# Kernel optimization log

Measured on AMD Instinct MI355X. Metric: run time of the kernel, lower is better.

## Reference

```python
import jax, jax.numpy as jnp
import numpy as np

H = 16      # how_many_heads
DH = 64     # dimension_of_head
D_K = 1024  # dimension_of_key (input dim); scaler = sqrt(D_K), faithful to source
NEG = -np.finfo(np.float32).max


def setup_inputs() -> dict:
    key0 = jax.random.key(0)
    ks = jax.random.split(key0, 8)
    B, S, D = 2, 2048, 1024
    query = jax.random.normal(ks[0], (B, S, D), dtype=jnp.float32)
    key_in = jax.random.normal(ks[1], (B, S, D), dtype=jnp.float32)
    value = jax.random.normal(ks[2], (B, S, D), dtype=jnp.float32)
    mask = jax.random.bernoulli(ks[3], 0.5, (B, S, S))  # bool, True = masked
    # nn.Linear(in, out, bias=False): y = x @ W^T with W:[out,in]; store [in,out] directly
    sc = 1.0 / np.sqrt(D)
    W_q = jax.random.normal(ks[4], (D, H * DH), dtype=jnp.float32) * sc
    W_k = jax.random.normal(ks[5], (D, H * DH), dtype=jnp.float32) * sc
    W_v = jax.random.normal(ks[6], (D, H * DH), dtype=jnp.float32) * sc
    W_o = jax.random.normal(ks[7], (H * DH, D), dtype=jnp.float32) * sc
    return {"query": query, "key": key_in, "value": value, "mask": mask,
            "W_q": W_q, "W_k": W_k, "W_v": W_v, "W_o": W_o}


def reference(query, key, value, mask, W_q, W_k, W_v, W_o):
    B, Sq, _ = query.shape
    # project and split heads: [B, S, H, DH] -> [B, H, S, DH]
    q = (query @ W_q).reshape(B, Sq, H, DH).transpose(0, 2, 1, 3)
    k = (key @ W_k).reshape(B, -1, H, DH).transpose(0, 2, 1, 3)
    v = (value @ W_v).reshape(B, -1, H, DH).transpose(0, 2, 1, 3)
    # scores: [B, H, Sq, Sk], scaled by sqrt(dimension_of_key)=sqrt(D_K)
    scores = jnp.einsum('bhqd,bhkd->bhqk', q, k) / np.float32(np.sqrt(D_K))
    # mask: [B, Sq, Sk] -> [B, H, Sq, Sk]; masked_fill with -finfo(float32).max
    scores = jnp.where(mask[:, None, :, :], NEG, scores)
    # FAITHFUL to source: softmax over dim=2 (the QUERY axis of the 4D tensor)
    attn = jax.nn.softmax(scores, axis=2)
    hidden = jnp.einsum('bhqk,bhkd->bhqd', attn, v)  # [B, H, Sq, DH]
    hidden = hidden.transpose(0, 2, 1, 3).reshape(B, Sq, H * DH) @ W_o
    return hidden, k, v
```

## Files before the change

kernel.cpp:

```cpp
#include <hip/hip_runtime.h>
#include <hip/hip_bf16.h>

#define BB 2
#define SS 2048
#define DD 1024
#define HH 16
#define DHH 64

#define SCLOG2E 0.045084221f

typedef unsigned short u16;
typedef unsigned int   u32;
typedef __bf16 bf16_t;
typedef bf16_t bf16x8 __attribute__((ext_vector_type(8)));
typedef u16    u16x8  __attribute__((ext_vector_type(8)));
typedef u32    u32x4v __attribute__((ext_vector_type(4)));
typedef float  f32x4  __attribute__((ext_vector_type(4)));

#define MFMA(a,b,c) __builtin_amdgcn_mfma_f32_16x16x32_bf16(a,b,c,0,0,0)

#define SW(c,r)  ((c) ^ ((r) & 7))
#define SW3(c,r) ((c) ^ ((r) & 3))

typedef __attribute__((address_space(1))) const unsigned int as1_u32;
typedef __attribute__((address_space(3))) unsigned int as3_u32;

__device__ __forceinline__ void gld16(const void* g, void* l){
  __builtin_amdgcn_global_load_lds((as1_u32*)g, (as3_u32*)l, 16, 0, 0);
}

__device__ __forceinline__ u16 f2bf(float f){
  u32 u = __builtin_bit_cast(u32, f);
  u32 r = (u + 0x7fffu + ((u >> 16) & 1u)) >> 16;
  return (u16)r;
}
__device__ __forceinline__ u16 nbf(float f){
  bf16_t b = (bf16_t)f;
  return __builtin_bit_cast(u16, b);
}
__device__ __forceinline__ float bf2f(u16 v){
  u32 u = ((u32)v) << 16;
  return __builtin_bit_cast(float, u);
}
__device__ __forceinline__ bf16x8 ldb8(const u16* p){
  return __builtin_bit_cast(bf16x8, *(const u16x8*)p);
}

__device__ __forceinline__ void stage64(const u16* __restrict__ g0, int stride,
                                        u16* lds0, int tid){
  int w = tid >> 6, lane = tid & 63;
  #pragma unroll
  for (int j = 0; j < 2; j++){
    int slot = j*256 + w*64 + lane;
    int row = slot >> 3, c = slot & 7;
    gld16(g0 + (size_t)row*stride + (SW(c,row) << 3),
          lds0 + (size_t)(j*256 + w*64)*8);
  }
}

__device__ __forceinline__ void stage32(const u16* __restrict__ g0, int stride,
                                        u16* lds0, int tid){
  int w = tid >> 6, lane = tid & 63;
  #pragma unroll
  for (int j = 0; j < 2; j++){
    int slot = j*256 + w*64 + lane;
    int row = slot >> 2, c = slot & 3;
    gld16(g0 + (size_t)row*stride + (SW3(c,row) << 3),
          lds0 + (size_t)(j*256 + w*64)*8);
  }
}

__global__ __launch_bounds__(256) void cvt3(const float* __restrict__ s0,
                                            const float* __restrict__ s1,
                                            const float* __restrict__ s2,
                                            u16* __restrict__ d0,
                                            u16* __restrict__ d1,
                                            u16* __restrict__ d2){
  const float* s = blockIdx.z == 0 ? s0 : (blockIdx.z == 1 ? s1 : s2);
  u16*         d = blockIdx.z == 0 ? d0 : (blockIdx.z == 1 ? d1 : d2);
  size_t i = ((size_t)blockIdx.x*256 + threadIdx.x) * 8;
  const float4* p = (const float4*)(s + i);
  float4 x = p[0], y = p[1];
  u16x8 u;
  u[0]=f2bf(x.x); u[1]=f2bf(x.y); u[2]=f2bf(x.z); u[3]=f2bf(x.w);
  u[4]=f2bf(y.x); u[5]=f2bf(y.y); u[6]=f2bf(y.z); u[7]=f2bf(y.w);
  *(u16x8*)(d + i) = u;
}

__global__ __launch_bounds__(256) void detect_mask(const u32* mw, u32* flag){
  __shared__ int fBig, fFloat;
  if (threadIdx.x == 0){ fBig = 0; fFloat = 0; }
  __syncthreads();
  for (int i = threadIdx.x; i < 4096; i += 256){
    u32 w = mw[i];
    if (w == 0x3f800000u) fFloat = 1;
    else if (w > 1u) fBig = 1;
  }
  __syncthreads();
  if (threadIdx.x == 0) *flag = fFloat ? 2u : (fBig ? 1u : 0u);
}

__global__ __launch_bounds__(256) void pack_mask(const void* __restrict__ mask,
                                                 const u32* __restrict__ flag,
                                                 u32* __restrict__ pm){
  int w = blockIdx.x * 256 + threadIdx.x;
  if (w >= BB*SS*(SS/32)) return;
  u32 f = *flag;
  size_t e0 = (size_t)w * 32;
  u32 bits = 0;
  if (f == 1u){
    const uchar4* mb = (const uchar4*)((const unsigned char*)mask + e0);
    #pragma unroll
    for (int j = 0; j < 8; j++){
      uchar4 v = mb[j];
      bits |= (v.x?1u:0u) << (4*j)   | (v.y?1u:0u) << (4*j+1)
            | (v.z?1u:0u) << (4*j+2) | (v.w?1u:0u) << (4*j+3);
    }
  } else if (f == 0u){
    const int4* mi = (const int4*)((const int*)mask + e0);
    #pragma unroll
    for (int j = 0; j < 8; j++){
      int4 v = mi[j];
      bits |= (v.x?1u:0u) << (4*j)   | (v.y?1u:0u) << (4*j+1)
            | (v.z?1u:0u) << (4*j+2) | (v.w?1u:0u) << (4*j+3);
    }
  } else {
    const float4* mf = (const float4*)((const float*)mask + e0);
    #pragma unroll
    for (int j = 0; j < 8; j++){
      float4 v = mf[j];
      bits |= (v.x!=0.f?1u:0u) << (4*j)   | (v.y!=0.f?1u:0u) << (4*j+1)
            | (v.z!=0.f?1u:0u) << (4*j+2) | (v.w!=0.f?1u:0u) << (4*j+3);
    }
  }
  pm[w] = bits;
}

__global__ __launch_bounds__(256) void prep_w(const float* __restrict__ W0,
                                              const float* __restrict__ W1,
                                              const float* __restrict__ W2,
                                              const float* __restrict__ W3,
                                              u16* __restrict__ Wt){
  const float* Ws[4] = {W0, W1, W2, W3};
  const float* W = Ws[blockIdx.z];
  float scl = (blockIdx.z == 0) ? SCLOG2E : 1.0f;
  u16* O = Wt + (size_t)blockIdx.z * DD * DD;
  __shared__ float tile[64][65];
  int kb = blockIdx.x * 64, nb = blockIdx.y * 64;
  int col = threadIdx.x & 63, rr = threadIdx.x >> 6;
  #pragma unroll
  for (int i = 0; i < 16; i++){
    int row = i*4 + rr;
    tile[row][col] = W[(size_t)(kb+row)*DD + nb + col];
  }
  __syncthreads();
  #pragma unroll
  for (int i = 0; i < 16; i++){
    int row = i*4 + rr;
    O[(size_t)(nb+row)*DD + kb + col] = f2bf(tile[col][row] * scl);
  }
}

struct GA { const u16* A; const u16* Bt; u16* Cb; float* Co; int mode; };

__global__ __launch_bounds__(256) void gemm32(GA a0, GA a1, GA a2){
  GA ga = blockIdx.z == 0 ? a0 : (blockIdx.z == 1 ? a1 : a2);
  __shared__ u16 As[2][128*32];
  __shared__ u16 Bs[2][128*32];
  int mb = blockIdx.x * 128, nb = blockIdx.y * 128;
  int tid = threadIdx.x, w = tid >> 6, lane = tid & 63, ln = lane & 15, g = lane >> 4;
  int wr = w >> 1, wc = w & 1;
  f32x4 acc[4][4];
  #pragma unroll
  for (int i = 0; i < 4; i++)
    #pragma unroll
    for (int j = 0; j < 4; j++) acc[i][j] = (f32x4){0,0,0,0};

  stage32(ga.A  + (size_t)mb*DD, DD, As[0], tid);
  stage32(ga.Bt + (size_t)nb*DD, DD, Bs[0], tid);
  __syncthreads();
  int buf = 0;
  for (int t = 0; t < 32; t++){
    if (t < 31){
      stage32(ga.A  + (size_t)mb*DD + (t+1)*32, DD, As[buf^1], tid);
      stage32(ga.Bt + (size_t)nb*DD + (t+1)*32, DD, Bs[buf^1], tid);
    }
    bf16x8 av[4], bv[4];
    #pragma unroll
    for (int mf = 0; mf < 4; mf++){
      int row = wr*64 + mf*16 + ln;
      av[mf] = ldb8(&As[buf][row*32 + (SW3(g,row) << 3)]);
    }
    #pragma unroll
    for (int nf = 0; nf < 4; nf++){
      int row = wc*64 + nf*16 + ln;
      bv[nf] = ldb8(&Bs[buf][row*32 + (SW3(g,row) << 3)]);
    }
    #pragma unroll
    for (int mf = 0; mf < 4; mf++)
      #pragma unroll
      for (int nf = 0; nf < 4; nf++)
        acc[mf][nf] = MFMA(av[mf], bv[nf], acc[mf][nf]);
    __syncthreads();
    buf ^= 1;
  }
  #pragma unroll
  for (int mf = 0; mf < 4; mf++){
    #pragma unroll
    for (int nf = 0; nf < 4; nf++){
      #pragma unroll
      for (int r = 0; r < 4; r++){
        int row = mb + wr*64 + mf*16 + g*4 + r;
        int col = nb + wc*64 + nf*16 + ln;
        float v = acc[mf][nf][r];
        if (ga.mode != 2)
          ga.Cb[(size_t)row*DD + col] = f2bf(v);
        if (ga.mode == 1){
          int b_ = row >> 11, s_ = row & (SS-1);
          int h_ = col >> 6,  d_ = col & 63;
          ga.Co[(((size_t)(b_*HH + h_))*SS + s_)*DHH + d_] = v;
        }
        if (ga.mode == 2)
          ga.Co[(size_t)row*DD + col] = v;
      }
    }
  }
}

__global__ __launch_bounds__(256) void pass1_sum(const u16* __restrict__ Qb,
                                                 const u16* __restrict__ Kb,
                                                 const u32* __restrict__ pm,
                                                 float* __restrict__ cO){
  __shared__ u16 Qst[2][64*64];
  int b = blockIdx.z, h = blockIdx.y;
  int kblk = blockIdx.x * 128;
  int tid = threadIdx.x, w = tid >> 6, lane = tid & 63, ln = lane & 15, g = lane >> 4;
  bf16x8 kf[2][2];
  #pragma unroll
  for (int f = 0; f < 2; f++){
    const u16* kp = Kb + ((size_t)b*SS + kblk + w*32 + f*16 + ln)*DD + h*DHH + g*8;
    kf[f][0] = ldb8(kp); kf[f][1] = ldb8(kp + 32);
  }
  float cr[2][4] = {{0,0,0,0},{0,0,0,0}};

  stage64(Qb + ((size_t)b*SS)*DD + h*DHH, DD, Qst[0], tid);
  __syncthreads();
  int buf = 0;
  int kwbase = (b*SS)*(SS/32) + (kblk >> 5) + w;
  for (int t = 0; t < 32; t++){
    if (t < 31) stage64(Qb + ((size_t)b*SS + (t+1)*64)*DD + h*DHH, DD, Qst[buf^1], tid);
    #pragma unroll
    for (int qc = 0; qc < 4; qc++){
      int row = qc*16 + ln;
      bf16x8 b0 = ldb8(&Qst[buf][row*64 + (SW(g,  row) << 3)]);
      bf16x8 b1 = ldb8(&Qst[buf][row*64 + (SW(g+4,row) << 3)]);
      int q = t*64 + qc*16 + ln;
      u32 mw = pm[(size_t)q*(SS/32) + kwbase];
      #pragma unroll
      for (int f = 0; f < 2; f++){
        f32x4 sf = {0,0,0,0};
        sf = MFMA(kf[f][0], b0, sf);
        sf = MFMA(kf[f][1], b1, sf);
        #pragma unroll
        for (int r = 0; r < 4; r++){
          float e = __builtin_amdgcn_exp2f(sf[r]);
          cr[f][r] += ((mw >> (f*16 + g*4 + r)) & 1u) ? 0.f : e;
        }
      }
    }
    __syncthreads();
    buf ^= 1;
  }
  #pragma unroll
  for (int f = 0; f < 2; f++)
    #pragma unroll
    for (int r = 0; r < 4; r++){
      #pragma unroll
      for (int msk = 1; msk < 16; msk <<= 1)
        cr[f][r] += __shfl_xor(cr[f][r], msk, 64);
    }
  if (ln == 0){
    #pragma unroll
    for (int f = 0; f < 2; f++)
      #pragma unroll
      for (int r = 0; r < 4; r++)
        cO[((size_t)b*HH + h)*SS + kblk + w*32 + f*16 + g*4 + r] = cr[f][r];
  }
}

__global__ __launch_bounds__(256) void scale_v(const u16* __restrict__ Vb,
                                               const float* __restrict__ cI,
                                               u16* __restrict__ Vt){
  int b = blockIdx.z, h = blockIdx.y;
  int st = blockIdx.x * 64;
  __shared__ u16 tile[64][72];
  int col = threadIdx.x & 63, rr = threadIdx.x >> 6;
  #pragma unroll
  for (int i = 0; i < 16; i++){
    int row = i*4 + rr;
    int s = st + row;
    float inv = 1.0f / cI[((size_t)b*HH + h)*SS + s];
    float v = bf2f(Vb[((size_t)b*SS + s)*DD + h*DHH + col]);
    tile[row][col] = f2bf(v * inv);
  }
  __syncthreads();
  int pc = ((col >> 2) & 3)*16 + (col >> 4)*4 + (col & 3);
  #pragma unroll
  for (int i = 0; i < 16; i++){
    int row = i*4 + rr;
    Vt[(((size_t)b*HH + h)*DHH + row)*SS + st + pc] = tile[col][row];
  }
}

__global__ __launch_bounds__(256) void pass2_pv(const u16* __restrict__ Qb,
                                                const u16* __restrict__ Kb,
                                                const u16* __restrict__ Vt,
                                                const u32* __restrict__ pm,
                                                u16* __restrict__ Hb){
  __shared__ u16 Kst[2][64*64];
  __shared__ u16 Vst[2][64*64];
  __shared__ u16 P[4][32*72];
  int b = blockIdx.z, h = blockIdx.y;
  int qt = blockIdx.x * 128;
  int tid = threadIdx.x, w = tid >> 6, lane = tid & 63, ln = lane & 15, g = lane >> 4;
  u16* Pw = &P[w][0];
  bf16x8 qf[2][2];
  #pragma unroll
  for (int f = 0; f < 2; f++){
    const u16* qp = Qb + ((size_t)b*SS + qt + w*32 + f*16 + ln)*DD + h*DHH + g*8;
    qf[f][0] = ldb8(qp); qf[f][1] = ldb8(qp + 32);
  }
  f32x4 acc[2][4];
  #pragma unroll
  for (int f = 0; f < 2; f++)
    #pragma unroll
    for (int d = 0; d < 4; d++) acc[f][d] = (f32x4){0,0,0,0};

  const u16* Kg  = Kb + ((size_t)b*SS)*DD + h*DHH;
  const u16* Vth = Vt + ((size_t)b*HH + h)*DHH*SS;

  stage64(Kg,  DD, Kst[0], tid);
  stage64(Vth, SS, Vst[0], tid);
  __syncthreads();
  int buf = 0;
  for (int t = 0; t < 32; t++){
    if (t < 31){
      stage64(Kg + (size_t)(t+1)*64*DD, DD, Kst[buf^1], tid);
      stage64(Vth + (t+1)*64,           SS, Vst[buf^1], tid);
    }
    u32 mlo[2], mhi[2];
    #pragma unroll
    for (int f = 0; f < 2; f++){
      const u32* pw = pm + ((size_t)b*SS + qt + w*32 + f*16 + ln)*(SS/32) + t*2;
      mlo[f] = pw[0]; mhi[f] = pw[1];
    }
    u32 pk[2][8];
    #pragma unroll
    for (int kc = 0; kc < 4; kc++){
      int row = kc*16 + ln;
      bf16x8 a0 = ldb8(&Kst[buf][row*64 + (SW(g,  row) << 3)]);
      bf16x8 a1 = ldb8(&Kst[buf][row*64 + (SW(g+4,row) << 3)]);
      #pragma unroll
      for (int f = 0; f < 2; f++){
        f32x4 sf = {0,0,0,0};
        sf = MFMA(a0, qf[f][0], sf);
        sf = MFMA(a1, qf[f][1], sf);
        u32 mword = (kc < 2) ? mlo[f] : mhi[f];
        int msh = (kc & 1) * 16 + g*4;
        float p0 = ((mword >> (msh+0)) & 1u) ? 0.f : __builtin_amdgcn_exp2f(sf[0]);
        float p1 = ((mword >> (msh+1)) & 1u) ? 0.f : __builtin_amdgcn_exp2f(sf[1]);
        float p2 = ((mword >> (msh+2)) & 1u) ? 0.f : __builtin_amdgcn_exp2f(sf[2]);
        float p3 = ((mword >> (msh+3)) & 1u) ? 0.f : __builtin_amdgcn_exp2f(sf[3]);
        pk[f][kc*2]   = (u32)nbf(p0) | ((u32)nbf(p1) << 16);
        pk[f][kc*2+1] = (u32)nbf(p2) | ((u32)nbf(p3) << 16);
      }
    }
    #pragma unroll
    for (int f = 0; f < 2; f++){
      u16* pr = &Pw[(f*16 + ln)*72 + g*16];
      *(u32x4v*)pr       = (u32x4v){pk[f][0], pk[f][1], pk[f][2], pk[f][3]};
      *(u32x4v*)(pr + 8) = (u32x4v){pk[f][4], pk[f][5], pk[f][6], pk[f][7]};
    }
    #pragma unroll
    for (int kh = 0; kh < 2; kh++){
      bf16x8 pa[2];
      #pragma unroll
      for (int f = 0; f < 2; f++)
        pa[f] = ldb8(&Pw[(f*16 + ln)*72 + kh*32 + g*8]);
      #pragma unroll
      for (int df = 0; df < 4; df++){
        int row = df*16 + ln;
        bf16x8 bv = ldb8(&Vst[buf][row*64 + (SW(kh*4+g, row) << 3)]);
        #pragma unroll
        for (int f = 0; f < 2; f++)
          acc[f][df] = MFMA(pa[f], bv, acc[f][df]);
      }
    }
    __syncthreads();
    buf ^= 1;
  }
  #pragma unroll
  for (int f = 0; f < 2; f++)
    #pragma unroll
    for (int df = 0; df < 4; df++)
      #pragma unroll
      for (int r = 0; r < 4; r++){
        int row = qt + w*32 + f*16 + g*4 + r;
        int col = h*DHH + df*16 + ln;
        Hb[((size_t)b*SS + row)*DD + col] = f2bf(acc[f][df][r]);
      }
}

extern "C" void kernel_launch(void* const* d_in, const int* in_sizes, int n_in,
                              void* d_out, int out_size, void* d_ws, size_t ws_size,
                              hipStream_t stream){
  (void)in_sizes; (void)n_in; (void)out_size; (void)ws_size;
  const float* query = (const float*)d_in[0];
  const float* key   = (const float*)d_in[1];
  const float* value = (const float*)d_in[2];
  const void*  mask  = d_in[3];
  const float* W_q = (const float*)d_in[4];
  const float* W_k = (const float*)d_in[5];
  const float* W_v = (const float*)d_in[6];
  const float* W_o = (const float*)d_in[7];

  float* out   = (float*)d_out;
  float* out_h = out;
  float* out_k = out   + (size_t)BB*HH*SS*DHH;
  float* out_v = out_k + (size_t)BB*HH*SS*DHH;

  char* w = (char*)d_ws;
  u16*   Wt  = (u16*)(w);
  u16*   Av  = (u16*)(w + (size_t)( 8u<<20));
  u16*   Qb  = (u16*)(w + (size_t)(16u<<20));
  u16*   Kb  = (u16*)(w + (size_t)(24u<<20));
  u16*   Vb  = (u16*)(w + (size_t)(32u<<20));
  u16*   Vt  = (u16*)(w + (size_t)(40u<<20));
  float* cS  = (float*)(w + (size_t)(48u<<20));
  u32*   pm  = (u32*)(w + (size_t)(48u<<20) + (512u<<10));
  u32*   flag= (u32*)(w + (size_t)(48u<<20) + (1664u<<10));
  u16*   Hb  = Av;
  u16*   Aq  = (u16*)out_h;
  u16*   Ak  = Aq + (size_t)BB*SS*DD;

  detect_mask<<<dim3(1), dim3(256), 0, stream>>>((const u32*)mask, flag);
  pack_mask<<<dim3(1024), dim3(256), 0, stream>>>(mask, flag, pm);
  prep_w<<<dim3(16,16,4), dim3(256), 0, stream>>>(W_q, W_k, W_v, W_o, Wt);

  cvt3<<<dim3(2048,1,3), dim3(256), 0, stream>>>(query, key, value, Aq, Ak, Av);

  GA gq = { Aq, Wt,             Qb, nullptr, 0 };
  GA gk = { Ak, Wt + 1*1048576, Kb, out_k,   1 };
  GA gv = { Av, Wt + 2*1048576, Vb, out_v,   1 };
  gemm32<<<dim3(32,8,3), dim3(256), 0, stream>>>(gq, gk, gv);

  pass1_sum<<<dim3(SS/128, HH, BB), dim3(256), 0, stream>>>(Qb, Kb, pm, cS);
  scale_v<<<dim3(SS/64, HH, BB), dim3(256), 0, stream>>>(Vb, cS, Vt);
  pass2_pv<<<dim3(SS/128, HH, BB), dim3(256), 0, stream>>>(Qb, Kb, Vt, pm, Hb);

  GA go = { Hb, Wt + 3*1048576, nullptr, out_h, 2 };
  gemm32<<<dim3(32,8,1), dim3(256), 0, stream>>>(go, go, go);
}
```

Baseline: 227.6 us.

## Halve per-wave tile in attention passes and keep P in registers

Both attention passes now give each wave 16 rows instead of 32, so the grid doubles to SS/64 blocks per head. In pass2 the exp'd probabilities are no longer written to and read back from a shared-memory P buffer. The score MFMA output layout is reused directly as the A operand of the PV MFMA, with the V transpose permutation in scale_v changed to match the new key ordering. This removes LDS traffic and the P buffer, raising occupancy and block count. The cost is that each K/V tile staged in shared memory is reused by half as many query rows, which doubles the global staging traffic.

```diff
diff --git a/kernel.cpp b/kernel.cpp
--- a/kernel.cpp
+++ b/kernel.cpp
@@ -233,20 +233,17 @@
                                                  float* __restrict__ cO){
   __shared__ u16 Qst[2][64*64];
   int b = blockIdx.z, h = blockIdx.y;
-  int kblk = blockIdx.x * 128;
+  int kblk = blockIdx.x * 64;
   int tid = threadIdx.x, w = tid >> 6, lane = tid & 63, ln = lane & 15, g = lane >> 4;
-  bf16x8 kf[2][2];
-  #pragma unroll
-  for (int f = 0; f < 2; f++){
-    const u16* kp = Kb + ((size_t)b*SS + kblk + w*32 + f*16 + ln)*DD + h*DHH + g*8;
-    kf[f][0] = ldb8(kp); kf[f][1] = ldb8(kp + 32);
-  }
-  float cr[2][4] = {{0,0,0,0},{0,0,0,0}};
+  const u16* kp = Kb + ((size_t)b*SS + kblk + w*16 + ln)*DD + h*DHH + g*8;
+  bf16x8 kf0 = ldb8(kp), kf1 = ldb8(kp + 32);
+  float cr[4] = {0,0,0,0};
 
   stage64(Qb + ((size_t)b*SS)*DD + h*DHH, DD, Qst[0], tid);
   __syncthreads();
   int buf = 0;
-  int kwbase = (b*SS)*(SS/32) + (kblk >> 5) + w;
+  size_t kword = (size_t)(b*SS)*(SS/32) + ((kblk + w*16) >> 5);
+  int ksh = (w & 1) * 16 + g*4;
   for (int t = 0; t < 32; t++){
     if (t < 31) stage64(Qb + ((size_t)b*SS + (t+1)*64)*DD + h*DHH, DD, Qst[buf^1], tid);
     #pragma unroll
@@ -255,36 +252,29 @@
       bf16x8 b0 = ldb8(&Qst[buf][row*64 + (SW(g,  row) << 3)]);
       bf16x8 b1 = ldb8(&Qst[buf][row*64 + (SW(g+4,row) << 3)]);
       int q = t*64 + qc*16 + ln;
-      u32 mw = pm[(size_t)q*(SS/32) + kwbase];
+      f32x4 sf = {0,0,0,0};
+      sf = MFMA(kf0, b0, sf);
+      sf = MFMA(kf1, b1, sf);
+      u32 mw = pm[(size_t)q*(SS/32) + kword];
       #pragma unroll
-      for (int f = 0; f < 2; f++){
-        f32x4 sf = {0,0,0,0};
-        sf = MFMA(kf[f][0], b0, sf);
-        sf = MFMA(kf[f][1], b1, sf);
-        #pragma unroll
-        for (int r = 0; r < 4; r++){
-          float e = __builtin_amdgcn_exp2f(sf[r]);
-          cr[f][r] += ((mw >> (f*16 + g*4 + r)) & 1u) ? 0.f : e;
-        }
+      for (int r = 0; r < 4; r++){
+        float e = __builtin_amdgcn_exp2f(sf[r]);
+        cr[r] += ((mw >> (ksh + r)) & 1u) ? 0.f : e;
       }
     }
     __syncthreads();
     buf ^= 1;
   }
   #pragma unroll
-  for (int f = 0; f < 2; f++)
-    #pragma unroll
-    for (int r = 0; r < 4; r++){
-      #pragma unroll
-      for (int msk = 1; msk < 16; msk <<= 1)
-        cr[f][r] += __shfl_xor(cr[f][r], msk, 64);
-    }
+  for (int r = 0; r < 4; r++){
+    #pragma unroll
+    for (int msk = 1; msk < 16; msk <<= 1)
+      cr[r] += __shfl_xor(cr[r], msk, 64);
+  }
   if (ln == 0){
     #pragma unroll
-    for (int f = 0; f < 2; f++)
-      #pragma unroll
-      for (int r = 0; r < 4; r++)
-        cO[((size_t)b*HH + h)*SS + kblk + w*32 + f*16 + g*4 + r] = cr[f][r];
+    for (int r = 0; r < 4; r++)
+      cO[((size_t)b*HH + h)*SS + kblk + w*16 + g*4 + r] = cr[r];
   }
 }
 
@@ -304,7 +294,7 @@
     tile[row][col] = f2bf(v * inv);
   }
   __syncthreads();
-  int pc = ((col >> 2) & 3)*16 + (col >> 4)*4 + (col & 3);
+  int pc = (col & 32) + ((col >> 2) & 3)*8 + ((col >> 4) & 1)*4 + (col & 3);
   #pragma unroll
   for (int i = 0; i < 16; i++){
     int row = i*4 + rr;
@@ -319,25 +309,19 @@
                                                 u16* __restrict__ Hb){
   __shared__ u16 Kst[2][64*64];
   __shared__ u16 Vst[2][64*64];
-  __shared__ u16 P[4][32*72];
   int b = blockIdx.z, h = blockIdx.y;
-  int qt = blockIdx.x * 128;
+  int qt = blockIdx.x * 64;
   int tid = threadIdx.x, w = tid >> 6, lane = tid & 63, ln = lane & 15, g = lane >> 4;
-  u16* Pw = &P[w][0];
-  bf16x8 qf[2][2];
-  #pragma unroll
-  for (int f = 0; f < 2; f++){
-    const u16* qp = Qb + ((size_t)b*SS + qt + w*32 + f*16 + ln)*DD + h*DHH + g*8;
-    qf[f][0] = ldb8(qp); qf[f][1] = ldb8(qp + 32);
-  }
-  f32x4 acc[2][4];
-  #pragma unroll
-  for (int f = 0; f < 2; f++)
-    #pragma unroll
-    for (int d = 0; d < 4; d++) acc[f][d] = (f32x4){0,0,0,0};
+  int qrow = qt + w*16 + ln;
+  const u16* qp = Qb + ((size_t)b*SS + qrow)*DD + h*DHH + g*8;
+  bf16x8 qf0 = ldb8(qp), qf1 = ldb8(qp + 32);
+  f32x4 acc[4];
+  #pragma unroll
+  for (int d = 0; d < 4; d++) acc[d] = (f32x4){0,0,0,0};
 
   const u16* Kg  = Kb + ((size_t)b*SS)*DD + h*DHH;
   const u16* Vth = Vt + ((size_t)b*HH + h)*DHH*SS;
+  const u32* pmrow = pm + ((size_t)b*SS + qrow)*(SS/32);
 
   stage64(Kg,  DD, Kst[0], tid);
   stage64(Vth, SS, Vst[0], tid);
@@ -348,67 +332,47 @@
       stage64(Kg + (size_t)(t+1)*64*DD, DD, Kst[buf^1], tid);
       stage64(Vth + (t+1)*64,           SS, Vst[buf^1], tid);
     }
-    u32 mlo[2], mhi[2];
-    #pragma unroll
-    for (int f = 0; f < 2; f++){
-      const u32* pw = pm + ((size_t)b*SS + qt + w*32 + f*16 + ln)*(SS/32) + t*2;
-      mlo[f] = pw[0]; mhi[f] = pw[1];
-    }
-    u32 pk[2][8];
+    u32 mlo = pmrow[t*2], mhi = pmrow[t*2 + 1];
+    u32 pk[8];
     #pragma unroll
     for (int kc = 0; kc < 4; kc++){
       int row = kc*16 + ln;
       bf16x8 a0 = ldb8(&Kst[buf][row*64 + (SW(g,  row) << 3)]);
       bf16x8 a1 = ldb8(&Kst[buf][row*64 + (SW(g+4,row) << 3)]);
-      #pragma unroll
-      for (int f = 0; f < 2; f++){
-        f32x4 sf = {0,0,0,0};
-        sf = MFMA(a0, qf[f][0], sf);
-        sf = MFMA(a1, qf[f][1], sf);
-        u32 mword = (kc < 2) ? mlo[f] : mhi[f];
-        int msh = (kc & 1) * 16 + g*4;
-        float p0 = ((mword >> (msh+0)) & 1u) ? 0.f : __builtin_amdgcn_exp2f(sf[0]);
-        float p1 = ((mword >> (msh+1)) & 1u) ? 0.f : __builtin_amdgcn_exp2f(sf[1]);
-        float p2 = ((mword >> (msh+2)) & 1u) ? 0.f : __builtin_amdgcn_exp2f(sf[2]);
-        float p3 = ((mword >> (msh+3)) & 1u) ? 0.f : __builtin_amdgcn_exp2f(sf[3]);
-        pk[f][kc*2]   = (u32)nbf(p0) | ((u32)nbf(p1) << 16);
-        pk[f][kc*2+1] = (u32)nbf(p2) | ((u32)nbf(p3) << 16);
-      }
-    }
-    #pragma unroll
-    for (int f = 0; f < 2; f++){
-      u16* pr = &Pw[(f*16 + ln)*72 + g*16];
-      *(u32x4v*)pr       = (u32x4v){pk[f][0], pk[f][1], pk[f][2], pk[f][3]};
-      *(u32x4v*)(pr + 8) = (u32x4v){pk[f][4], pk[f][5], pk[f][6], pk[f][7]};
+      f32x4 sf = {0,0,0,0};
+      sf = MFMA(a0, qf0, sf);
+      sf = MFMA(a1, qf1, sf);
+      u32 mword = (kc < 2) ? mlo : mhi;
+      int msh = (kc & 1) * 16 + g*4;
+      float p0 = ((mword >> (msh+0)) & 1u) ? 0.f : __builtin_amdgcn_exp2f(sf[0]);
+      float p1 = ((mword >> (msh+1)) & 1u) ? 0.f : __builtin_amdgcn_exp2f(sf[1]);
+      float p2 = ((mword >> (msh+2)) & 1u) ? 0.f : __builtin_amdgcn_exp2f(sf[2]);
+      float p3 = ((mword >> (msh+3)) & 1u) ? 0.f : __builtin_amdgcn_exp2f(sf[3]);
+      pk[kc*2]   = (u32)nbf(p0) | ((u32)nbf(p1) << 16);
+      pk[kc*2+1] = (u32)nbf(p2) | ((u32)nbf(p3) << 16);
     }
     #pragma unroll
     for (int kh = 0; kh < 2; kh++){
-      bf16x8 pa[2];
-      #pragma unroll
-      for (int f = 0; f < 2; f++)
-        pa[f] = ldb8(&Pw[(f*16 + ln)*72 + kh*32 + g*8]);
+      bf16x8 pa = __builtin_bit_cast(bf16x8,
+        (u32x4v){pk[4*kh], pk[4*kh+1], pk[4*kh+2], pk[4*kh+3]});
       #pragma unroll
       for (int df = 0; df < 4; df++){
         int row = df*16 + ln;
         bf16x8 bv = ldb8(&Vst[buf][row*64 + (SW(kh*4+g, row) << 3)]);
-        #pragma unroll
-        for (int f = 0; f < 2; f++)
-          acc[f][df] = MFMA(pa[f], bv, acc[f][df]);
+        acc[df] = MFMA(pa, bv, acc[df]);
       }
     }
     __syncthreads();
     buf ^= 1;
   }
   #pragma unroll
-  for (int f = 0; f < 2; f++)
-    #pragma unroll
-    for (int df = 0; df < 4; df++)
-      #pragma unroll
-      for (int r = 0; r < 4; r++){
-        int row = qt + w*32 + f*16 + g*4 + r;
-        int col = h*DHH + df*16 + ln;
-        Hb[((size_t)b*SS + row)*DD + col] = f2bf(acc[f][df][r]);
-      }
+  for (int df = 0; df < 4; df++)
+    #pragma unroll
+    for (int r = 0; r < 4; r++){
+      int row = qt + w*16 + g*4 + r;
+      int col = h*DHH + df*16 + ln;
+      Hb[((size_t)b*SS + row)*DD + col] = f2bf(acc[df][r]);
+    }
 }
 
 extern "C" void kernel_launch(void* const* d_in, const int* in_sizes, int n_in,
@@ -454,9 +418,9 @@
   GA gv = { Av, Wt + 2*1048576, Vb, out_v,   1 };
   gemm32<<<dim3(32,8,3), dim3(256), 0, stream>>>(gq, gk, gv);
 
-  pass1_sum<<<dim3(SS/128, HH, BB), dim3(256), 0, stream>>>(Qb, Kb, pm, cS);
+  pass1_sum<<<dim3(SS/64, HH, BB), dim3(256), 0, stream>>>(Qb, Kb, pm, cS);
   scale_v<<<dim3(SS/64, HH, BB), dim3(256), 0, stream>>>(Vb, cS, Vt);
-  pass2_pv<<<dim3(SS/128, HH, BB), dim3(256), 0, stream>>>(Qb, Kb, Vt, pm, Hb);
+  pass2_pv<<<dim3(SS/64, HH, BB), dim3(256), 0, stream>>>(Qb, Kb, Vt, pm, Hb);
 
   GA go = { Hb, Wt + 3*1048576, nullptr, out_h, 2 };
   gemm32<<<dim3(32,8,1), dim3(256), 0, stream>>>(go, go, go);
```

Measured after the change: 245.5 us. +7.9%, slower.

## Feed P directly from registers via permuted V layout; swizzle block order

Applied to the files above, without the earlier changes.

Removes the per-wave LDS round trip for the probability tile in pass2 by changing the column permutation of the transposed V, so each lane's packed P registers already form the MFMA A operand. Both attention passes also remap block indices so neighbouring blocks span different heads and batches, which should spread cache and channel traffic. The permutation in scale_v has to match the implied k ordering exactly, otherwise results are wrong.

```diff
diff --git a/kernel.cpp b/kernel.cpp
--- a/kernel.cpp
+++ b/kernel.cpp
@@ -232,8 +232,11 @@
                                                  const u32* __restrict__ pm,
                                                  float* __restrict__ cO){
   __shared__ u16 Qst[2][64*64];
-  int b = blockIdx.z, h = blockIdx.y;
-  int kblk = blockIdx.x * 128;
+  int flat = blockIdx.x + (SS/128)*(blockIdx.y + HH*blockIdx.z);
+  int sw = (flat & 7)*64 + (flat >> 3);
+  int kblk = (sw & 15) * 128;
+  int rest = sw >> 4;
+  int h = rest & 15, b = rest >> 4;
   int tid = threadIdx.x, w = tid >> 6, lane = tid & 63, ln = lane & 15, g = lane >> 4;
   bf16x8 kf[2][2];
   #pragma unroll
@@ -246,7 +249,7 @@
   stage64(Qb + ((size_t)b*SS)*DD + h*DHH, DD, Qst[0], tid);
   __syncthreads();
   int buf = 0;
-  int kwbase = (b*SS)*(SS/32) + (kblk >> 5) + w;
+  size_t kwbase = (size_t)(b*SS)*(SS/32) + (kblk >> 5) + w;
   for (int t = 0; t < 32; t++){
     if (t < 31) stage64(Qb + ((size_t)b*SS + (t+1)*64)*DD + h*DHH, DD, Qst[buf^1], tid);
     #pragma unroll
@@ -304,7 +307,7 @@
     tile[row][col] = f2bf(v * inv);
   }
   __syncthreads();
-  int pc = ((col >> 2) & 3)*16 + (col >> 4)*4 + (col & 3);
+  int pc = (col & 32) + ((col >> 2) & 3)*8 + ((col >> 4) & 1)*4 + (col & 3);
   #pragma unroll
   for (int i = 0; i < 16; i++){
     int row = i*4 + rr;
@@ -319,11 +322,12 @@
                                                 u16* __restrict__ Hb){
   __shared__ u16 Kst[2][64*64];
   __shared__ u16 Vst[2][64*64];
-  __shared__ u16 P[4][32*72];
-  int b = blockIdx.z, h = blockIdx.y;
-  int qt = blockIdx.x * 128;
+  int flat = blockIdx.x + (SS/128)*(blockIdx.y + HH*blockIdx.z);
+  int sw = (flat & 7)*64 + (flat >> 3);
+  int qt = (sw & 15) * 128;
+  int rest = sw >> 4;
+  int h = rest & 15, b = rest >> 4;
   int tid = threadIdx.x, w = tid >> 6, lane = tid & 63, ln = lane & 15, g = lane >> 4;
-  u16* Pw = &P[w][0];
   bf16x8 qf[2][2];
   #pragma unroll
   for (int f = 0; f < 2; f++){
@@ -338,6 +342,10 @@
 
   const u16* Kg  = Kb + ((size_t)b*SS)*DD + h*DHH;
   const u16* Vth = Vt + ((size_t)b*HH + h)*DHH*SS;
+  const u32* pmr[2];
+  #pragma unroll
+  for (int f = 0; f < 2; f++)
+    pmr[f] = pm + ((size_t)b*SS + qt + w*32 + f*16 + ln)*(SS/32);
 
   stage64(Kg,  DD, Kst[0], tid);
   stage64(Vth, SS, Vst[0], tid);
@@ -350,10 +358,7 @@
     }
     u32 mlo[2], mhi[2];
     #pragma unroll
-    for (int f = 0; f < 2; f++){
-      const u32* pw = pm + ((size_t)b*SS + qt + w*32 + f*16 + ln)*(SS/32) + t*2;
-      mlo[f] = pw[0]; mhi[f] = pw[1];
-    }
+    for (int f = 0; f < 2; f++){ mlo[f] = pmr[f][t*2]; mhi[f] = pmr[f][t*2+1]; }
     u32 pk[2][8];
     #pragma unroll
     for (int kc = 0; kc < 4; kc++){
@@ -376,17 +381,12 @@
       }
     }
     #pragma unroll
-    for (int f = 0; f < 2; f++){
-      u16* pr = &Pw[(f*16 + ln)*72 + g*16];
-      *(u32x4v*)pr       = (u32x4v){pk[f][0], pk[f][1], pk[f][2], pk[f][3]};
-      *(u32x4v*)(pr + 8) = (u32x4v){pk[f][4], pk[f][5], pk[f][6], pk[f][7]};
-    }
-    #pragma unroll
     for (int kh = 0; kh < 2; kh++){
       bf16x8 pa[2];
       #pragma unroll
       for (int f = 0; f < 2; f++)
-        pa[f] = ldb8(&Pw[(f*16 + ln)*72 + kh*32 + g*8]);
+        pa[f] = __builtin_bit_cast(bf16x8,
+          (u32x4v){pk[f][4*kh], pk[f][4*kh+1], pk[f][4*kh+2], pk[f][4*kh+3]});
       #pragma unroll
       for (int df = 0; df < 4; df++){
         int row = df*16 + ln;
```

Result: faster. 216.4 us (-4.9%).
